# Kernel optimization log

Measured on AMD Instinct MI355X. Metric: run time of the kernel, lower is better.

## Reference

```python
import jax, jax.numpy as jnp
import numpy as np

B, N, C = 16, 4096, 512
FR = 2          # fr_ratio
NH = 8          # num_heads
CF = C // FR    # 256, q/k/v projection dim
HD = (C // NH) // FR  # 32, per-head dim after fr reduction
EPS = 1e-4


def _abs_clamp(t):
    # sign(t) * clamp(|t|, 1e-4, 1e4), as in the torch module's abs_clamp
    return jnp.sign(t) * jnp.clip(jnp.abs(t), 1e-4, 1e4)


def setup_inputs() -> dict:
    key = jax.random.key(0)
    ks = jax.random.split(key, 8)
    s = 0.02  # trunc_normal_(std=0.02) init scale
    return {
        "query": jax.random.normal(ks[0], (B, N, C), jnp.float32),
        "Wq": jax.random.normal(ks[1], (CF, C), jnp.float32) * s,
        "bq": jnp.zeros((CF,), jnp.float32),
        "Wk": jax.random.normal(ks[2], (CF, C), jnp.float32) * s,
        "bk": jnp.zeros((CF,), jnp.float32),
        "Wv": jax.random.normal(ks[3], (CF, C), jnp.float32) * s,
        "bv": jnp.zeros((CF,), jnp.float32),
        "Wo": jax.random.normal(ks[4], (C, CF), jnp.float32) * s,
        "bo": jnp.zeros((C,), jnp.float32),
        "Wse1": jax.random.normal(ks[5], (C // 2, C), jnp.float32) * s,
        "Wse2": jax.random.normal(ks[6], (C, C // 2), jnp.float32) * s,
        "H": 64,
        "W": 64,
    }


def reference(query, Wq, bq, Wk, bk, Wv, bv, Wo, bo, Wse1, Wse2, H, W):
    Bq, Nq, Cq = query.shape  # N == H*W
    # --- squeeze-excitation gate: mean over tokens -> 2-layer MLP -> sigmoid
    se = jnp.mean(query, axis=1)                                   # [B, C]
    se = jax.nn.sigmoid(jax.nn.relu(se @ Wse1.T) @ Wse2.T)         # [B, C]

    # --- q/k/v projections (sr_ratio=1: k/v from full-length query)
    q = jax.nn.relu(query @ Wq.T + bq).reshape(Bq, Nq, NH, HD)     # [B,N,h,d]
    k = jax.nn.relu(query @ Wk.T + bk).reshape(Bq, Nq, NH, HD)
    v = (query @ Wv.T + bv).reshape(Bq, Nq, NH, HD)

    # --- cosFormer-style 2D positional feature maps
    c = jnp.pi / 2
    idx = jnp.arange(Nq)
    a = (c * (idx // W).astype(query.dtype) / H)[None, :, None, None]  # row angle
    b = (c * (idx % W).astype(query.dtype) / W)[None, :, None, None]   # col angle
    q_ = jnp.concatenate([q * jnp.cos(a), q * jnp.sin(a),
                          q * jnp.cos(b), q * jnp.sin(b)], axis=-1)    # [B,N,h,4d]
    k_ = jnp.concatenate([k * jnp.cos(a), k * jnp.sin(a),
                          k * jnp.cos(b), k * jnp.sin(b)], axis=-1)    # sr_ratio=1 -> same angles

    # --- linear attention: kv state then q lookup, with abs-clamping
    kv = _abs_clamp(jnp.einsum('bnhf,bnhd->bhfd', k_, v))          # [B,h,4d,d]
    k_sum = jnp.sum(k_, axis=1, keepdims=True)                     # [B,1,h,4d]
    z = _abs_clamp(1.0 / (jnp.sum(q_ * k_sum, axis=-1) + EPS))     # [B,N,h]
    out = _abs_clamp(jnp.einsum('bnhf,bhfd->bnhd', q_, kv))        # [B,N,h,d]
    out = _abs_clamp(out * z[..., None])

    # --- output projection + SE residual gating
    out = _abs_clamp(out.reshape(Bq, Nq, CF) @ Wo.T + bo)          # [B,N,C]
    out = _abs_clamp(out + out * se[:, None, :])
    return out
```

## Files before the change

kernel.cpp:

```cpp
#include <hip/hip_runtime.h>
#include <math.h>

#define B_   16
#define N_   4096
#define C_   512
#define CF_  256
#define NH_  8
#define HD_  32
#define FHD_ 128
#define BN_  (B_ * N_)
#define EPS_ 1e-4f
#define PI2F 1.5707963267948966f

typedef _Float16 half8 __attribute__((ext_vector_type(8)));
typedef _Float16 half4 __attribute__((ext_vector_type(4)));
typedef float f32x4 __attribute__((ext_vector_type(4)));
typedef unsigned short u16x8 __attribute__((ext_vector_type(8)));

__device__ __forceinline__ float abs_clamp(float t) {
    float a = fminf(fmaxf(fabsf(t), 1e-4f), 1e4f);
    return t > 0.f ? a : (t < 0.f ? -a : 0.f);
}
__device__ __forceinline__ void gld16(const void* g, void* l) {
    __builtin_amdgcn_global_load_lds(
        (const __attribute__((address_space(1))) void*)g,
        (__attribute__((address_space(3))) void*)l, 16, 0, 0);
}

__global__ __launch_bounds__(256) void se_sum_kernel(const float* __restrict__ q,
                                                     float* __restrict__ sesum,
                                                     _Float16* __restrict__ q16) {
    int b = blockIdx.x, chunk = blockIdx.y;
    int t = threadIdx.x;
    int c = (t & 127) * 4;
    int tok0 = chunk * 64 + (t >> 7) * 32;
    const float* p = q + ((size_t)b * N_ + tok0) * C_ + c;
    _Float16* o = q16 + ((size_t)b * N_ + tok0) * C_ + c;
    float a0 = 0.f, a1 = 0.f, a2 = 0.f, a3 = 0.f;
#pragma unroll 4
    for (int n = 0; n < 32; n++) {
        float4 v = *(const float4*)(p + (size_t)n * C_);
        a0 += v.x; a1 += v.y; a2 += v.z; a3 += v.w;
        half4 hv;
        hv[0] = (_Float16)v.x; hv[1] = (_Float16)v.y;
        hv[2] = (_Float16)v.z; hv[3] = (_Float16)v.w;
        *(half4*)(o + (size_t)n * C_) = hv;
    }
    atomicAdd(&sesum[b * C_ + c + 0], a0);
    atomicAdd(&sesum[b * C_ + c + 1], a1);
    atomicAdd(&sesum[b * C_ + c + 2], a2);
    atomicAdd(&sesum[b * C_ + c + 3], a3);
}

__global__ __launch_bounds__(256) void se_gate_kernel(const float* __restrict__ sesum,
                                                      const float* __restrict__ Wse1,
                                                      const float* __restrict__ Wse2,
                                                      float* __restrict__ segate) {
    __shared__ float sm[C_];
    __shared__ float hm[C_ / 2];
    int b = blockIdx.x, t = threadIdx.x;
    sm[t]       = sesum[b * C_ + t]       * (1.f / N_);
    sm[t + 256] = sesum[b * C_ + t + 256] * (1.f / N_);
    __syncthreads();
    {
        const float* w = Wse1 + (size_t)t * C_;
        float acc = 0.f;
        for (int c2 = 0; c2 < C_; c2++) acc += sm[c2] * w[c2];
        hm[t] = fmaxf(acc, 0.f);
    }
    __syncthreads();
    for (int r = 0; r < 2; r++) {
        int c2 = t + r * 256;
        const float* w2 = Wse2 + (size_t)c2 * (C_ / 2);
        float a2 = 0.f;
        for (int j = 0; j < C_ / 2; j++) a2 += hm[j] * w2[j];
        segate[b * C_ + c2] = 1.f / (1.f + expf(-a2));
    }
}

__global__ __launch_bounds__(256) void convert_w(const float* __restrict__ Wq,
                                                 const float* __restrict__ Wk,
                                                 const float* __restrict__ Wv,
                                                 const float* __restrict__ Wo,
                                                 _Float16* __restrict__ wcat,
                                                 _Float16* __restrict__ wo16) {
    int i = blockIdx.x * 256 + threadIdx.x;
    if (i < 768 * 512) {
        int r = i >> 9, c = i & 511;
        float w = (r < 256) ? Wq[(size_t)r * 512 + c]
                : (r < 512) ? Wk[(size_t)(r - 256) * 512 + c]
                            : Wv[(size_t)(r - 512) * 512 + c];
        wcat[i] = (_Float16)w;
    } else {
        int j = i - 768 * 512;
        wo16[j] = (_Float16)Wo[j];
    }
}

__global__ __launch_bounds__(256) void gemm_qkv(
    const _Float16* __restrict__ A16, const _Float16* __restrict__ Bw,
    const float* __restrict__ bq, const float* __restrict__ bk, const float* __restrict__ bv,
    _Float16* __restrict__ Oq, _Float16* __restrict__ kT, _Float16* __restrict__ vT) {
    constexpr int K = 512;
    constexpr int NITER = K / 32;

    __shared__ __align__(16) unsigned short As[3][128 * 32];
    __shared__ __align__(16) unsigned short Bs[3][128 * 32];

    const int t = threadIdx.x;
    const int did = blockIdx.x + 6 * blockIdx.y;
    const int lid = (did & 7) * 384 + (did >> 3);
    const int bx = lid % 6;
    const int Mb = (lid / 6) * 128;
    const int nrow0 = bx * 128;

    const int lane = t & 63;
    const int wv = t >> 6;
    const int mq = (wv >> 1) * 64;
    const int nq = (wv & 1) * 64;
    const int mrow = lane & 15;
    const int kq = lane >> 4;
    const int fragoff = mrow * 32 + ((kq ^ ((mrow >> 1) & 3)) * 8);

    const unsigned char *asrc0, *asrc1, *bsrc0, *bsrc1;
    int off0, off1;
    {
        int cid0 = t, cid1 = t + 256;
        int m0 = cid0 >> 2, c0 = (cid0 & 3) ^ ((m0 >> 1) & 3);
        int m1 = cid1 >> 2, c1 = (cid1 & 3) ^ ((m1 >> 1) & 3);
        asrc0 = (const unsigned char*)(A16 + (size_t)(Mb + m0) * K + c0 * 8);
        asrc1 = (const unsigned char*)(A16 + (size_t)(Mb + m1) * K + c1 * 8);
        bsrc0 = (const unsigned char*)(Bw + (size_t)(nrow0 + m0) * K + c0 * 8);
        bsrc1 = (const unsigned char*)(Bw + (size_t)(nrow0 + m1) * K + c1 * 8);
        off0 = cid0 * 8;
        off1 = cid1 * 8;
    }

    f32x4 acc[4][4];
#pragma unroll
    for (int mi = 0; mi < 4; mi++)
#pragma unroll
        for (int ni = 0; ni < 4; ni++) acc[mi][ni] = (f32x4){0.f, 0.f, 0.f, 0.f};

    gld16(asrc0, &As[0][off0]);
    gld16(asrc1, &As[0][off1]);
    gld16(bsrc0, &Bs[0][off0]);
    gld16(bsrc1, &Bs[0][off1]);
    gld16(asrc0 + 64, &As[1][off0]);
    gld16(asrc1 + 64, &As[1][off1]);
    gld16(bsrc0 + 64, &Bs[1][off0]);
    gld16(bsrc1 + 64, &Bs[1][off1]);

    int cur = 0;
#pragma unroll 1
    for (int it = 0; it < NITER; ++it) {
        if (it + 1 < NITER) {
            asm volatile("s_waitcnt vmcnt(4)" ::: "memory");
        } else {
            asm volatile("s_waitcnt vmcnt(0)" ::: "memory");
        }
        __builtin_amdgcn_sched_barrier(0);
        __builtin_amdgcn_s_barrier();
        if (it + 2 < NITER) {
            int nb = cur + 2; if (nb >= 3) nb -= 3;
            gld16(asrc0 + (it + 2) * 64, &As[nb][off0]);
            gld16(asrc1 + (it + 2) * 64, &As[nb][off1]);
            gld16(bsrc0 + (it + 2) * 64, &Bs[nb][off0]);
            gld16(bsrc1 + (it + 2) * 64, &Bs[nb][off1]);
        }

        half8 ah[4], bh[4];
#pragma unroll
        for (int mi = 0; mi < 4; mi++)
            ah[mi] = *(const half8*)&As[cur][(mq + mi * 16) * 32 + fragoff];
#pragma unroll
        for (int ni = 0; ni < 4; ni++)
            bh[ni] = *(const half8*)&Bs[cur][(nq + ni * 16) * 32 + fragoff];
#pragma unroll
        for (int mi = 0; mi < 4; mi++)
#pragma unroll
            for (int ni = 0; ni < 4; ni++)
                acc[mi][ni] = __builtin_amdgcn_mfma_f32_16x16x32_f16(ah[mi], bh[ni], acc[mi][ni], 0, 0, 0);

        cur = (cur == 2) ? 0 : cur + 1;
    }

#pragma unroll
    for (int ni = 0; ni < 4; ni++) {
        int gc = nrow0 + nq + ni * 16 + mrow;
        int mat = gc >> 8;
        int col = gc & 255;
        float bb = (mat == 0 ? bq : mat == 1 ? bk : bv)[col];
        if (mat == 0) {
#pragma unroll
            for (int mi = 0; mi < 4; mi++)
#pragma unroll
                for (int r = 0; r < 4; r++) {
                    int m = Mb + mq + mi * 16 + kq * 4 + r;
                    float v2 = fmaxf(acc[mi][ni][r] + bb, 0.f);
                    Oq[(size_t)m * CF_ + col] = (_Float16)v2;
                }
        } else {
            _Float16* OT = (mat == 1) ? kT : vT;
#pragma unroll
            for (int mi = 0; mi < 4; mi++) {
                int m0r = Mb + mq + mi * 16 + kq * 4;
                half4 hv;
#pragma unroll
                for (int r = 0; r < 4; r++) {
                    float v2 = acc[mi][ni][r] + bb;
                    if (mat == 1) v2 = fmaxf(v2, 0.f);
                    hv[r] = (_Float16)v2;
                }
                *(half4*)&OT[(size_t)col * BN_ + m0r] = hv;
            }
        }
    }
}

__global__ __launch_bounds__(256) void gemm_out(
    const _Float16* __restrict__ A16, const _Float16* __restrict__ Bw,
    const float* __restrict__ bo, const float* __restrict__ sg,
    float* __restrict__ Of) {
    constexpr int K = 256;
    constexpr int NITER = K / 32;

    __shared__ __align__(16) unsigned short As[3][128 * 32];
    __shared__ __align__(16) unsigned short Bs[3][128 * 32];

    const int t = threadIdx.x;
    const int did = blockIdx.x + 4 * blockIdx.y;
    const int lid = (did & 7) * 256 + (did >> 3);
    const int bx = lid & 3;
    const int Mb = (lid >> 2) * 128;
    const int nrow0 = bx * 128;

    const int lane = t & 63;
    const int wv = t >> 6;
    const int mq = (wv >> 1) * 64;
    const int nq = (wv & 1) * 64;
    const int mrow = lane & 15;
    const int kq = lane >> 4;
    const int fragoff = mrow * 32 + ((kq ^ ((mrow >> 1) & 3)) * 8);

    const unsigned char *asrc0, *asrc1, *bsrc0, *bsrc1;
    int off0, off1;
    {
        int cid0 = t, cid1 = t + 256;
        int m0 = cid0 >> 2, c0 = (cid0 & 3) ^ ((m0 >> 1) & 3);
        int m1 = cid1 >> 2, c1 = (cid1 & 3) ^ ((m1 >> 1) & 3);
        asrc0 = (const unsigned char*)(A16 + (size_t)(Mb + m0) * K + c0 * 8);
        asrc1 = (const unsigned char*)(A16 + (size_t)(Mb + m1) * K + c1 * 8);
        bsrc0 = (const unsigned char*)(Bw + (size_t)(nrow0 + m0) * K + c0 * 8);
        bsrc1 = (const unsigned char*)(Bw + (size_t)(nrow0 + m1) * K + c1 * 8);
        off0 = cid0 * 8;
        off1 = cid1 * 8;
    }

    f32x4 acc[4][4];
#pragma unroll
    for (int mi = 0; mi < 4; mi++)
#pragma unroll
        for (int ni = 0; ni < 4; ni++) acc[mi][ni] = (f32x4){0.f, 0.f, 0.f, 0.f};

    gld16(asrc0, &As[0][off0]);
    gld16(asrc1, &As[0][off1]);
    gld16(bsrc0, &Bs[0][off0]);
    gld16(bsrc1, &Bs[0][off1]);
    gld16(asrc0 + 64, &As[1][off0]);
    gld16(asrc1 + 64, &As[1][off1]);
    gld16(bsrc0 + 64, &Bs[1][off0]);
    gld16(bsrc1 + 64, &Bs[1][off1]);

    int cur = 0;
#pragma unroll 1
    for (int it = 0; it < NITER; ++it) {
        if (it + 1 < NITER) {
            asm volatile("s_waitcnt vmcnt(4)" ::: "memory");
        } else {
            asm volatile("s_waitcnt vmcnt(0)" ::: "memory");
        }
        __builtin_amdgcn_sched_barrier(0);
        __builtin_amdgcn_s_barrier();
        if (it + 2 < NITER) {
            int nb = cur + 2; if (nb >= 3) nb -= 3;
            gld16(asrc0 + (it + 2) * 64, &As[nb][off0]);
            gld16(asrc1 + (it + 2) * 64, &As[nb][off1]);
            gld16(bsrc0 + (it + 2) * 64, &Bs[nb][off0]);
            gld16(bsrc1 + (it + 2) * 64, &Bs[nb][off1]);
        }

        half8 ah[4], bh[4];
#pragma unroll
        for (int mi = 0; mi < 4; mi++)
            ah[mi] = *(const half8*)&As[cur][(mq + mi * 16) * 32 + fragoff];
#pragma unroll
        for (int ni = 0; ni < 4; ni++)
            bh[ni] = *(const half8*)&Bs[cur][(nq + ni * 16) * 32 + fragoff];
#pragma unroll
        for (int mi = 0; mi < 4; mi++)
#pragma unroll
            for (int ni = 0; ni < 4; ni++)
                acc[mi][ni] = __builtin_amdgcn_mfma_f32_16x16x32_f16(ah[mi], bh[ni], acc[mi][ni], 0, 0, 0);

        cur = (cur == 2) ? 0 : cur + 1;
    }

    int b = Mb >> 12;
#pragma unroll
    for (int ni = 0; ni < 4; ni++) {
        int gc = nrow0 + nq + ni * 16 + mrow;
        float bb = bo[gc];
        float gv = sg[b * C_ + gc];
#pragma unroll
        for (int mi = 0; mi < 4; mi++)
#pragma unroll
            for (int r = 0; r < 4; r++) {
                int m = Mb + mq + mi * 16 + kq * 4 + r;
                float v2 = abs_clamp(acc[mi][ni][r] + bb);
                v2 = abs_clamp(v2 * (1.f + gv));
                Of[(size_t)m * C_ + gc] = v2;
            }
    }
}

__global__ __launch_bounds__(256) void kv_mfma_kernel(const _Float16* __restrict__ kin,
                                                      const _Float16* __restrict__ vin,
                                                      float* __restrict__ kvout,
                                                      float* __restrict__ ksum) {
    __shared__ __align__(16) unsigned short Ah[128 * 128];
    __shared__ __align__(16) unsigned short Bh[48 * 128];

    const int t = threadIdx.x;
    const int c8 = blockIdx.x;
    const int h = blockIdx.y, b = blockIdx.z;
    const int dp = t & 31;
    const int oct = t >> 5;

    {
        int r = 32 + (t >> 4);
        int c = t & 15;
        unsigned short fill = (r == 32) ? (unsigned short)0x3C00 : (unsigned short)0;
        u16x8 z = {fill, fill, fill, fill, fill, fill, fill, fill};
        *(u16x8*)&Bh[r * 128 + ((c ^ (r & 7)) * 8)] = z;
    }

    float cbv[8], sbv[8];
#pragma unroll
    for (int i = 0; i < 8; i++) {
        float ang = (PI2F / 64.f) * (float)(oct * 8 + i);
        cbv[i] = cosf(ang);
        sbv[i] = sinf(ang);
    }

    const int lane = t & 63;
    const int wv = t >> 6;
    const int mrow = lane & 15;
    const int kq = lane >> 4;

    f32x4 acc[2][3];
#pragma unroll
    for (int mi = 0; mi < 2; mi++)
#pragma unroll
        for (int ni = 0; ni < 3; ni++) acc[mi][ni] = (f32x4){0.f, 0.f, 0.f, 0.f};

    int offAa[4], offAb[4];
#pragma unroll
    for (int tvar = 0; tvar < 4; tvar++) {
        int f = tvar * 32 + dp;
        offAa[tvar] = f * 128 + ((oct ^ (f & 7)) * 8);
        offAb[tvar] = f * 128 + (((oct + 8) ^ (f & 7)) * 8);
    }
    const int offBa = dp * 128 + ((oct ^ (dp & 7)) * 8);
    const int offBb = dp * 128 + (((oct + 8) ^ (dp & 7)) * 8);

    const size_t colbase = (size_t)(h * HD_ + dp) * BN_ + (size_t)b * N_;

    half8 kk[4][2], vv[4][2];
    {
        const _Float16* kp0 = kin + colbase + c8 * 512 + oct * 8;
        const _Float16* vp0 = vin + colbase + c8 * 512 + oct * 8;
#pragma unroll
        for (int ch = 0; ch < 4; ch++) {
            kk[ch][0] = *(const half8*)(kp0 + ch * 128);
            kk[ch][1] = *(const half8*)(kp0 + ch * 128 + 64);
            vv[ch][0] = *(const half8*)(vp0 + ch * 128);
            vv[ch][1] = *(const half8*)(vp0 + ch * 128 + 64);
        }
    }

#pragma unroll
    for (int ch = 0; ch < 4; ch++) {
        const int n0 = c8 * 512 + ch * 128;
        const int rr = n0 >> 6;
        float ca0 = cosf((PI2F / 64.f) * (float)rr),       sa0 = sinf((PI2F / 64.f) * (float)rr);
        float ca1 = cosf((PI2F / 64.f) * (float)(rr + 1)), sa1 = sinf((PI2F / 64.f) * (float)(rr + 1));

        float ka[8], kb[8];
#pragma unroll
        for (int i = 0; i < 8; i++) { ka[i] = (float)kk[ch][0][i]; kb[i] = (float)kk[ch][1][i]; }

        __syncthreads();

#pragma unroll
        for (int tvar = 0; tvar < 4; tvar++) {
            half8 ha, hb;
#pragma unroll
            for (int i = 0; i < 8; i++) {
                float fa = (tvar == 0) ? ca0 : (tvar == 1) ? sa0 : (tvar == 2) ? cbv[i] : sbv[i];
                float fb = (tvar == 0) ? ca1 : (tvar == 1) ? sa1 : (tvar == 2) ? cbv[i] : sbv[i];
                ha[i] = (_Float16)(ka[i] * fa);
                hb[i] = (_Float16)(kb[i] * fb);
            }
            *(half8*)&Ah[offAa[tvar]] = ha;
            *(half8*)&Ah[offAb[tvar]] = hb;
        }
        *(half8*)&Bh[offBa] = vv[ch][0];
        *(half8*)&Bh[offBb] = vv[ch][1];
        __syncthreads();

#pragma unroll
        for (int s = 0; s < 4; s++) {
            int koct = s * 4 + kq;
            half8 ah[2], bh[3];
#pragma unroll
            for (int mi = 0; mi < 2; mi++) {
                int f = (wv * 2 + mi) * 16 + mrow;
                ah[mi] = *(const half8*)&Ah[f * 128 + ((koct ^ (f & 7)) * 8)];
            }
#pragma unroll
            for (int ni = 0; ni < 3; ni++) {
                int nr = ni * 16 + mrow;
                bh[ni] = *(const half8*)&Bh[nr * 128 + ((koct ^ (nr & 7)) * 8)];
            }
#pragma unroll
            for (int mi = 0; mi < 2; mi++)
#pragma unroll
                for (int ni = 0; ni < 3; ni++)
                    acc[mi][ni] = __builtin_amdgcn_mfma_f32_16x16x32_f16(ah[mi], bh[ni], acc[mi][ni], 0, 0, 0);
        }
    }

    float* kvp = kvout + (size_t)(b * NH_ + h) * FHD_ * HD_;
    float* ksp = ksum + (size_t)(b * NH_ + h) * FHD_;
#pragma unroll
    for (int mi = 0; mi < 2; mi++) {
        int mt = wv * 2 + mi;
#pragma unroll
        for (int r = 0; r < 4; r++) {
            int f = mt * 16 + kq * 4 + r;
            atomicAdd(&kvp[(size_t)mrow * FHD_ + f], acc[mi][0][r]);
            atomicAdd(&kvp[(size_t)(16 + mrow) * FHD_ + f], acc[mi][1][r]);
            if (mrow == 0) atomicAdd(&ksp[f], acc[mi][2][r]);
        }
    }
}

__global__ __launch_bounds__(256) void attn_kernel(const _Float16* __restrict__ qbuf,
                                                   const float* __restrict__ kvin,
                                                   const float* __restrict__ ksum,
                                                   _Float16* __restrict__ ob) {
    __shared__ __align__(16) unsigned short Aq[128 * 40];
    __shared__ __align__(16) unsigned short Bk[48 * 128];
    __shared__ __align__(16) float tS[128][4];
    __shared__ float zS[128];

    const int chunk = blockIdx.x;
    const int h = blockIdx.y, b = blockIdx.z;
    const int t = threadIdx.x;
    const int n0 = chunk * 128;

    {
        const float* kvp = kvin + ((size_t)(b * NH_ + h)) * (HD_ * FHD_);
        int d = t >> 3;
        int c0 = (t & 7) * 2;
#pragma unroll
        for (int cc = 0; cc < 2; cc++) {
            int c = c0 + cc;
            const float* src = kvp + (size_t)d * FHD_ + c * 8;
            half8 hv;
#pragma unroll
            for (int i = 0; i < 8; i++) hv[i] = (_Float16)abs_clamp(src[i]);
            *(half8*)&Bk[d * 128 + ((c ^ (d & 7)) * 8)] = hv;
        }
        if (t < 16) {
            const float* ks = ksum + ((size_t)(b * NH_ + h)) * FHD_ + t * 8;
            half8 hv;
#pragma unroll
            for (int i = 0; i < 8; i++) hv[i] = (_Float16)ks[i];
            *(half8*)&Bk[32 * 128 + (t * 8)] = hv;
        } else {
            int idx = t - 16;
            int r = 33 + (idx >> 4), c = idx & 15;
            half8 z = {};
            *(half8*)&Bk[r * 128 + ((c ^ (r & 7)) * 8)] = z;
        }
    }
    {
        int tok = t >> 1, hf = t & 1;
        const _Float16* qp = qbuf + ((size_t)b * N_ + n0 + tok) * CF_ + h * HD_ + hf * 16;
        half8 a0 = *(const half8*)qp;
        half8 a1 = *(const half8*)(qp + 8);
        *(half8*)&Aq[tok * 40 + hf * 16] = a0;
        *(half8*)&Aq[tok * 40 + hf * 16 + 8] = a1;
    }
    if (t < 128) {
        int n = n0 + t;
        float aa = (PI2F / 64.f) * (float)(n >> 6);
        float ab = (PI2F / 64.f) * (float)(n & 63);
        tS[t][0] = cosf(aa); tS[t][1] = sinf(aa);
        tS[t][2] = cosf(ab); tS[t][3] = sinf(ab);
    }
    __syncthreads();

    const int lane = t & 63;
    const int wv = t >> 6;
    const int mrow = lane & 15;
    const int kq = lane >> 4;

    half8 ah[2];
#pragma unroll
    for (int mi = 0; mi < 2; mi++)
        ah[mi] = *(const half8*)&Aq[(wv * 32 + mi * 16 + mrow) * 40 + kq * 8];

    f32x4 acc[4][2][3];
#pragma unroll
    for (int tt = 0; tt < 4; tt++)
#pragma unroll
        for (int mi = 0; mi < 2; mi++)
#pragma unroll
            for (int ni = 0; ni < 3; ni++) acc[tt][mi][ni] = (f32x4){0.f, 0.f, 0.f, 0.f};

#pragma unroll
    for (int tt = 0; tt < 4; tt++) {
        half8 bh[3];
        int cpos = tt * 4 + kq;
#pragma unroll
        for (int ni = 0; ni < 3; ni++) {
            int row = ni * 16 + mrow;
            bh[ni] = *(const half8*)&Bk[row * 128 + ((cpos ^ (row & 7)) * 8)];
        }
#pragma unroll
        for (int mi = 0; mi < 2; mi++)
#pragma unroll
            for (int ni = 0; ni < 3; ni++)
                acc[tt][mi][ni] = __builtin_amdgcn_mfma_f32_16x16x32_f16(ah[mi], bh[ni], acc[tt][mi][ni], 0, 0, 0);
    }

    if (mrow == 0) {
#pragma unroll
        for (int mi = 0; mi < 2; mi++)
#pragma unroll
            for (int r = 0; r < 4; r++) {
                int tok = wv * 32 + mi * 16 + kq * 4 + r;
                float4 tv = *(const float4*)&tS[tok][0];
                float zraw = tv.x * acc[0][mi][2][r] + tv.y * acc[1][mi][2][r]
                           + tv.z * acc[2][mi][2][r] + tv.w * acc[3][mi][2][r];
                zS[tok] = abs_clamp(1.f / (zraw + EPS_));
            }
    }
    __syncthreads();

#pragma unroll
    for (int mi = 0; mi < 2; mi++) {
#pragma unroll
        for (int r = 0; r < 4; r++) {
            int tok = wv * 32 + mi * 16 + kq * 4 + r;
            float4 tv = *(const float4*)&tS[tok][0];
            float z = zS[tok];
            float v0 = tv.x * acc[0][mi][0][r] + tv.y * acc[1][mi][0][r]
                     + tv.z * acc[2][mi][0][r] + tv.w * acc[3][mi][0][r];
            float v1 = tv.x * acc[0][mi][1][r] + tv.y * acc[1][mi][1][r]
                     + tv.z * acc[2][mi][1][r] + tv.w * acc[3][mi][1][r];
            v0 = abs_clamp(abs_clamp(v0) * z);
            v1 = abs_clamp(abs_clamp(v1) * z);
            size_t base = ((size_t)b * N_ + n0 + tok) * CF_ + h * HD_;
            ob[base + mrow] = (_Float16)v0;
            ob[base + 16 + mrow] = (_Float16)v1;
        }
    }
}

extern "C" void kernel_launch(void* const* d_in, const int* in_sizes, int n_in,
                              void* d_out, int out_size, void* d_ws, size_t ws_size,
                              hipStream_t stream) {
    (void)in_sizes; (void)n_in; (void)out_size; (void)ws_size;
    const float* query = (const float*)d_in[0];
    const float* Wq = (const float*)d_in[1];
    const float* bq = (const float*)d_in[2];
    const float* Wk = (const float*)d_in[3];
    const float* bk = (const float*)d_in[4];
    const float* Wv = (const float*)d_in[5];
    const float* bv = (const float*)d_in[6];
    const float* Wo = (const float*)d_in[7];
    const float* bo = (const float*)d_in[8];
    const float* Wse1 = (const float*)d_in[9];
    const float* Wse2 = (const float*)d_in[10];
    float* out = (float*)d_out;

    unsigned char* ws = (unsigned char*)d_ws;
    const size_t MB = 1024ull * 1024ull;
    _Float16* q16 = (_Float16*)(ws + 0);
    _Float16* ob  = (_Float16*)(ws + 0);
    _Float16* qb  = (_Float16*)(ws + 64 * MB);
    _Float16* kbT = (_Float16*)(ws + 96 * MB);
    _Float16* vbT = (_Float16*)(ws + 128 * MB);
    _Float16* wcat = (_Float16*)(ws + 160 * MB);
    _Float16* wo16 = (_Float16*)(ws + 160 * MB + 786432);
    float* kvb = (float*)(ws + 161 * MB);
    float* ksb = (float*)(ws + 163 * MB);
    float* ssb = (float*)(ws + 163 * MB + 65536);
    float* sgb = (float*)(ws + 163 * MB + 98304);

    hipMemsetAsync(kvb, 0, 2097152 + 65536 + 32768, stream);

    convert_w<<<2048, 256, 0, stream>>>(Wq, Wk, Wv, Wo, wcat, wo16);
    se_sum_kernel<<<dim3(B_, 64), 256, 0, stream>>>(query, ssb, q16);
    se_gate_kernel<<<B_, 256, 0, stream>>>(ssb, Wse1, Wse2, sgb);
    gemm_qkv<<<dim3(6, 512), 256, 0, stream>>>(q16, wcat, bq, bk, bv, qb, kbT, vbT);
    kv_mfma_kernel<<<dim3(8, NH_, B_), 256, 0, stream>>>(kbT, vbT, kvb, ksb);
    attn_kernel<<<dim3(32, NH_, B_), 256, 0, stream>>>(qb, kvb, ksb, ob);
    gemm_out<<<dim3(4, 512), 256, 0, stream>>>(ob, wo16, bo, sgb, out);
}
```

Measured before the change: 525.9 us.

## Replace atomic kv accumulation with per-slice partials plus a reduction kernel

The kv-state kernel now splits the sequence into 16 slices of 256 tokens instead of 8 slices of 512, and writes per-slice partial kv and k_sum tiles to workspace with plain stores. A new reduce kernel sums the 16 partials and writes the transposed kv layout. This removes global float atomics and the large memset, and doubles block count. The LDS layout also changes from XOR swizzle to a padded stride of 136. In exchange there is an extra launch plus a write and read of the partials. The partials reuse the q16 workspace region, which is safe only if q16 is dead by then.

```diff
diff --git a/kernel.cpp b/kernel.cpp
--- a/kernel.cpp
+++ b/kernel.cpp
@@ -324,12 +324,13 @@
     }
 }
 
-__global__ __launch_bounds__(256) void kv_mfma_kernel(const _Float16* __restrict__ kin,
-                                                      const _Float16* __restrict__ vin,
-                                                      float* __restrict__ kvout,
-                                                      float* __restrict__ ksum) {
-    __shared__ __align__(16) unsigned short Ah[128 * 128];
-    __shared__ __align__(16) unsigned short Bh[48 * 128];
+#define AST 136
+__global__ __launch_bounds__(256) void kv_partial_kernel(const _Float16* __restrict__ kin,
+                                                         const _Float16* __restrict__ vin,
+                                                         float* __restrict__ pkv,
+                                                         float* __restrict__ pks) {
+    __shared__ __align__(16) unsigned short Ah[128 * AST];
+    __shared__ __align__(16) unsigned short Bh[48 * AST];
 
     const int t = threadIdx.x;
     const int c8 = blockIdx.x;
@@ -342,7 +343,7 @@
         int c = t & 15;
         unsigned short fill = (r == 32) ? (unsigned short)0x3C00 : (unsigned short)0;
         u16x8 z = {fill, fill, fill, fill, fill, fill, fill, fill};
-        *(u16x8*)&Bh[r * 128 + ((c ^ (r & 7)) * 8)] = z;
+        *(u16x8*)&Bh[r * AST + c * 8] = z;
     }
 
     float cbv[8], sbv[8];
@@ -364,34 +365,22 @@
 #pragma unroll
         for (int ni = 0; ni < 3; ni++) acc[mi][ni] = (f32x4){0.f, 0.f, 0.f, 0.f};
 
-    int offAa[4], offAb[4];
-#pragma unroll
-    for (int tvar = 0; tvar < 4; tvar++) {
-        int f = tvar * 32 + dp;
-        offAa[tvar] = f * 128 + ((oct ^ (f & 7)) * 8);
-        offAb[tvar] = f * 128 + (((oct + 8) ^ (f & 7)) * 8);
-    }
-    const int offBa = dp * 128 + ((oct ^ (dp & 7)) * 8);
-    const int offBb = dp * 128 + (((oct + 8) ^ (dp & 7)) * 8);
-
     const size_t colbase = (size_t)(h * HD_ + dp) * BN_ + (size_t)b * N_;
-
-    half8 kk[4][2], vv[4][2];
-    {
-        const _Float16* kp0 = kin + colbase + c8 * 512 + oct * 8;
-        const _Float16* vp0 = vin + colbase + c8 * 512 + oct * 8;
-#pragma unroll
-        for (int ch = 0; ch < 4; ch++) {
-            kk[ch][0] = *(const half8*)(kp0 + ch * 128);
-            kk[ch][1] = *(const half8*)(kp0 + ch * 128 + 64);
-            vv[ch][0] = *(const half8*)(vp0 + ch * 128);
-            vv[ch][1] = *(const half8*)(vp0 + ch * 128 + 64);
-        }
-    }
-
-#pragma unroll
-    for (int ch = 0; ch < 4; ch++) {
-        const int n0 = c8 * 512 + ch * 128;
+    const _Float16* kp0 = kin + colbase + c8 * 256 + oct * 8;
+    const _Float16* vp0 = vin + colbase + c8 * 256 + oct * 8;
+
+    half8 kk[2][2], vv[2][2];
+#pragma unroll
+    for (int ch = 0; ch < 2; ch++) {
+        kk[ch][0] = *(const half8*)(kp0 + ch * 128);
+        kk[ch][1] = *(const half8*)(kp0 + ch * 128 + 64);
+        vv[ch][0] = *(const half8*)(vp0 + ch * 128);
+        vv[ch][1] = *(const half8*)(vp0 + ch * 128 + 64);
+    }
+
+#pragma unroll
+    for (int ch = 0; ch < 2; ch++) {
+        const int n0 = c8 * 256 + ch * 128;
         const int rr = n0 >> 6;
         float ca0 = cosf((PI2F / 64.f) * (float)rr),       sa0 = sinf((PI2F / 64.f) * (float)rr);
         float ca1 = cosf((PI2F / 64.f) * (float)(rr + 1)), sa1 = sinf((PI2F / 64.f) * (float)(rr + 1));
@@ -404,6 +393,7 @@
 
 #pragma unroll
         for (int tvar = 0; tvar < 4; tvar++) {
+            int f = tvar * 32 + dp;
             half8 ha, hb;
 #pragma unroll
             for (int i = 0; i < 8; i++) {
@@ -412,26 +402,26 @@
                 ha[i] = (_Float16)(ka[i] * fa);
                 hb[i] = (_Float16)(kb[i] * fb);
             }
-            *(half8*)&Ah[offAa[tvar]] = ha;
-            *(half8*)&Ah[offAb[tvar]] = hb;
-        }
-        *(half8*)&Bh[offBa] = vv[ch][0];
-        *(half8*)&Bh[offBb] = vv[ch][1];
+            *(half8*)&Ah[f * AST + oct * 8] = ha;
+            *(half8*)&Ah[f * AST + 64 + oct * 8] = hb;
+        }
+        *(half8*)&Bh[dp * AST + oct * 8] = vv[ch][0];
+        *(half8*)&Bh[dp * AST + 64 + oct * 8] = vv[ch][1];
         __syncthreads();
 
 #pragma unroll
         for (int s = 0; s < 4; s++) {
-            int koct = s * 4 + kq;
+            int coff = (s * 4 + kq) * 8;
             half8 ah[2], bh[3];
 #pragma unroll
             for (int mi = 0; mi < 2; mi++) {
                 int f = (wv * 2 + mi) * 16 + mrow;
-                ah[mi] = *(const half8*)&Ah[f * 128 + ((koct ^ (f & 7)) * 8)];
+                ah[mi] = *(const half8*)&Ah[f * AST + coff];
             }
 #pragma unroll
             for (int ni = 0; ni < 3; ni++) {
                 int nr = ni * 16 + mrow;
-                bh[ni] = *(const half8*)&Bh[nr * 128 + ((koct ^ (nr & 7)) * 8)];
+                bh[ni] = *(const half8*)&Bh[nr * AST + coff];
             }
 #pragma unroll
             for (int mi = 0; mi < 2; mi++)
@@ -441,18 +431,45 @@
         }
     }
 
-    float* kvp = kvout + (size_t)(b * NH_ + h) * FHD_ * HD_;
-    float* ksp = ksum + (size_t)(b * NH_ + h) * FHD_;
+    const int bh = b * NH_ + h;
+    float* pv = pkv + ((size_t)c8 * 128 + bh) * (FHD_ * HD_);
+    float* ps = pks + ((size_t)c8 * 128 + bh) * FHD_;
 #pragma unroll
     for (int mi = 0; mi < 2; mi++) {
         int mt = wv * 2 + mi;
 #pragma unroll
         for (int r = 0; r < 4; r++) {
             int f = mt * 16 + kq * 4 + r;
-            atomicAdd(&kvp[(size_t)mrow * FHD_ + f], acc[mi][0][r]);
-            atomicAdd(&kvp[(size_t)(16 + mrow) * FHD_ + f], acc[mi][1][r]);
-            if (mrow == 0) atomicAdd(&ksp[f], acc[mi][2][r]);
-        }
+            pv[(size_t)f * HD_ + mrow] = acc[mi][0][r];
+            pv[(size_t)f * HD_ + 16 + mrow] = acc[mi][1][r];
+            if (mrow == 0) ps[f] = acc[mi][2][r];
+        }
+    }
+}
+
+__global__ __launch_bounds__(256) void kv_reduce_kernel(const float* __restrict__ pkv,
+                                                        const float* __restrict__ pks,
+                                                        float* __restrict__ kvout,
+                                                        float* __restrict__ ksum) {
+    const int bh = blockIdx.x;
+    const int part = blockIdx.y;
+    const int t = threadIdx.x;
+#pragma unroll
+    for (int i = 0; i < 2; i++) {
+        int e = t + (part * 2 + i) * 256;
+        float s = 0.f;
+#pragma unroll 4
+        for (int sl = 0; sl < 16; sl++)
+            s += pkv[((size_t)sl * 128 + bh) * (FHD_ * HD_) + e];
+        int f = e >> 5, d = e & 31;
+        kvout[(size_t)bh * (FHD_ * HD_) + (size_t)d * FHD_ + f] = s;
+    }
+    if (part == 0 && t < 128) {
+        float s = 0.f;
+#pragma unroll 4
+        for (int sl = 0; sl < 16; sl++)
+            s += pks[((size_t)sl * 128 + bh) * FHD_ + t];
+        ksum[bh * FHD_ + t] = s;
     }
 }
 
@@ -601,6 +618,8 @@
     unsigned char* ws = (unsigned char*)d_ws;
     const size_t MB = 1024ull * 1024ull;
     _Float16* q16 = (_Float16*)(ws + 0);
+    float*    pkv = (float*)(ws + 0);
+    float*    pks = (float*)(ws + 32 * MB);
     _Float16* ob  = (_Float16*)(ws + 0);
     _Float16* qb  = (_Float16*)(ws + 64 * MB);
     _Float16* kbT = (_Float16*)(ws + 96 * MB);
@@ -612,13 +631,14 @@
     float* ssb = (float*)(ws + 163 * MB + 65536);
     float* sgb = (float*)(ws + 163 * MB + 98304);
 
-    hipMemsetAsync(kvb, 0, 2097152 + 65536 + 32768, stream);
+    hipMemsetAsync(ssb, 0, 32768, stream);
 
     convert_w<<<2048, 256, 0, stream>>>(Wq, Wk, Wv, Wo, wcat, wo16);
     se_sum_kernel<<<dim3(B_, 64), 256, 0, stream>>>(query, ssb, q16);
     se_gate_kernel<<<B_, 256, 0, stream>>>(ssb, Wse1, Wse2, sgb);
     gemm_qkv<<<dim3(6, 512), 256, 0, stream>>>(q16, wcat, bq, bk, bv, qb, kbT, vbT);
-    kv_mfma_kernel<<<dim3(8, NH_, B_), 256, 0, stream>>>(kbT, vbT, kvb, ksb);
+    kv_partial_kernel<<<dim3(16, NH_, B_), 256, 0, stream>>>(kbT, vbT, pkv, pks);
+    kv_reduce_kernel<<<dim3(128, 8), 256, 0, stream>>>(pkv, pks, kvb, ksb);
     attn_kernel<<<dim3(32, NH_, B_), 256, 0, stream>>>(qb, kvb, ksb, ob);
     gemm_out<<<dim3(4, 512), 256, 0, stream>>>(ob, wo16, bo, sgb, out);
 }
```

New measurement: 499.8 us. 5.0% less time.
